# Optimization experiments

Hardware: AMD Instinct MI355X
Metric: run time of the kernel (lower is better)

The kernel has to match this reference:

```python
import jax, jax.numpy as jnp
import numpy as np

NUM_HEADS = 16
EPS = 1e-12  # torch F.normalize default eps


def _l2norm(t):
    n = jnp.linalg.norm(t, axis=-1, keepdims=True)
    return t / jnp.maximum(n, EPS)


def setup_inputs() -> dict:
    key = jax.random.key(0)
    ks = jax.random.split(key, 5)
    N, C, d = 16, 1024, 1024
    x = jax.random.normal(ks[0], (N, C, d), dtype=jnp.float32)
    Wq = jax.random.normal(ks[1], (d, d), dtype=jnp.float32) * 0.02
    Wk = jax.random.normal(ks[2], (d, d), dtype=jnp.float32) * 0.02
    Wv = jax.random.normal(ks[3], (d, d), dtype=jnp.float32) * 0.02
    Wo = jax.random.normal(ks[4], (d, d), dtype=jnp.float32) * 0.02
    norm_const = 0.5 * jnp.ones((1, NUM_HEADS, 1, 1), dtype=jnp.float32)
    return {"x": x, "Wq": Wq, "Wk": Wk, "Wv": Wv, "Wo": Wo, "norm_const": norm_const}


def reference(x, Wq, Wk, Wv, Wo, norm_const):
    # attn_type='cosine', causal=False branch of Attention.forward
    N, C, d = x.shape
    H = NUM_HEADS
    hd = d // H
    # torch nn.Linear(bias=False): y = x @ W.T ; split heads -> [N, H, C, hd]
    def proj(W):
        return (x @ W.T).reshape(N, C, H, hd).transpose(0, 2, 1, 3)
    q = _l2norm(proj(Wq))
    k = _l2norm(proj(Wk))
    v = proj(Wv)
    # values = values / C ** sigmoid(norm_const)  (per-head scalar)
    v = v / jnp.power(jnp.float32(C), jax.nn.sigmoid(norm_const))
    # linear-attention reordering: q @ (k^T @ v); kv is [N, H, hd, hd]
    kv = jnp.einsum('nhcd,nhce->nhde', k, v)
    attn = jnp.einsum('nhcd,nhde->nhce', q, kv)
    out = attn.transpose(0, 2, 1, 3).reshape(N, C, d)
    return out @ Wo.T
```

## Files before the change

kernel.cpp:

```cpp
#include <hip/hip_runtime.h>
#include <stdint.h>

typedef __attribute__((ext_vector_type(4))) float f32x4;
typedef __attribute__((ext_vector_type(8))) short bf16x8;
typedef __attribute__((ext_vector_type(4))) unsigned short u16x4;
typedef __attribute__((ext_vector_type(4))) unsigned int u32x4;

typedef __attribute__((address_space(3))) char lds_t;
typedef const __attribute__((address_space(1))) char gmem_t;

__device__ __forceinline__ float bf2f(unsigned short u) {
  union { unsigned int u; float f; } a; a.u = ((unsigned int)u) << 16; return a.f;
}
__device__ __forceinline__ unsigned short f2bf(float f) {
  union { float f; unsigned int u; } a; a.f = f;
  unsigned int r = a.u + 0x7fffu + ((a.u >> 16) & 1u);
  return (unsigned short)(r >> 16);
}

__global__ void cvt_kernel(const float* __restrict__ in, unsigned short* __restrict__ out, int n) {
  int i = (blockIdx.x * blockDim.x + threadIdx.x) * 8;
  if (i >= n) return;
  const f32x4 a = *(const f32x4*)(in + i);
  const f32x4 b = *(const f32x4*)(in + i + 4);
  alignas(16) unsigned short o[8];
#pragma unroll
  for (int k = 0; k < 4; ++k) { o[k] = f2bf(a[k]); o[4 + k] = f2bf(b[k]); }
  *(u32x4*)(out + i) = *(const u32x4*)o;
}

__global__ void cvtw_kernel(const float* __restrict__ W0, const float* __restrict__ W1,
                            const float* __restrict__ W2, const float* __restrict__ W3,
                            unsigned short* __restrict__ wqkv, unsigned short* __restrict__ wob) {
  const int s = blockIdx.y;
  const float* in = (s == 0) ? W0 : (s == 1) ? W1 : (s == 2) ? W2 : W3;
  unsigned short* out = (s < 3) ? (wqkv + s * 1048576) : wob;
  int i = (blockIdx.x * blockDim.x + threadIdx.x) * 8;
  const f32x4 a = *(const f32x4*)(in + i);
  const f32x4 b = *(const f32x4*)(in + i + 4);
  alignas(16) unsigned short o[8];
#pragma unroll
  for (int k = 0; k < 4; ++k) { o[k] = f2bf(a[k]); o[4 + k] = f2bf(b[k]); }
  *(u32x4*)(out + i) = *(const u32x4*)o;
}

template<int GX, int MODE>
__global__ __launch_bounds__(512, 2) void gemm256(
    const unsigned short* __restrict__ A, const unsigned short* __restrict__ B,
    void* __restrict__ O0, void* __restrict__ O1, void* __restrict__ O2,
    const float* __restrict__ nc)
{
  constexpr int K = 1024;
  constexpr int NT = K / 64;
  constexpr int NWG = GX * 64;
  constexpr int CPX = NWG >> 3;
  const int p = blockIdx.y * GX + blockIdx.x;
  const int lid = (p & 7) * CPX + (p >> 3);
  const int bm0 = (lid / GX) * 256;
  const int bn0 = (lid % GX) * 256;
  const int t = threadIdx.x;
  const int l = t & 63;
  const int w = t >> 6;
  const int wm = w >> 2;
  const int wn = w & 3;

  __shared__ char smem[131072];

  const int srow = t >> 3;
  const int schunk = t & 7;
  const int sck = schunk ^ (srow & 7);

#define STAGE_A(so_, kt_, lam_)                                                                  \
  __builtin_amdgcn_global_load_lds(                                                             \
      (gmem_t*)(A + (long long)(bm0 + (lam_) * 64 + srow) * K + (kt_) * 64 + sck * 8),          \
      (lds_t*)(smem + (so_) + ((lam_) * 64 + srow) * 128 + schunk * 16), 16, 0, 0)
#define STAGE_B(so_, kt_, lam_)                                                                  \
  __builtin_amdgcn_global_load_lds(                                                             \
      (gmem_t*)(B + (long long)(bn0 + (lam_) * 64 + srow) * K + (kt_) * 64 + sck * 8),          \
      (lds_t*)(smem + (so_) + 32768 + ((lam_) * 64 + srow) * 128 + schunk * 16), 16, 0, 0)

  const int xr = l & 7;
  const int chalf = l >> 4;
  int aoff[8], boff[4];
#pragma unroll
  for (int fr = 0; fr < 8; ++fr) aoff[fr] = (wm * 128 + fr * 16 + (l & 15)) * 128;
#pragma unroll
  for (int fc = 0; fc < 4; ++fc) boff[fc] = 32768 + (wn * 64 + fc * 16 + (l & 15)) * 128;

  f32x4 acc[8][4];
#pragma unroll
  for (int i = 0; i < 8; ++i)
#pragma unroll
    for (int j = 0; j < 4; ++j) acc[i][j] = f32x4{0.f, 0.f, 0.f, 0.f};

#pragma unroll
  for (int lam = 0; lam < 4; ++lam) STAGE_A(0, 0, lam);
#pragma unroll
  for (int lam = 0; lam < 4; ++lam) STAGE_B(0, 0, lam);
#pragma unroll
  for (int lam = 0; lam < 4; ++lam) STAGE_B(65536, 1, lam);
  asm volatile("s_waitcnt vmcnt(4)" ::: "memory");
  __builtin_amdgcn_s_barrier();
  __builtin_amdgcn_sched_barrier(0);

  for (int u = 0; u < NT; ++u) {
    const int slot = (u & 1) << 16;
    const int nslot = slot ^ 65536;
    bf16x8 bv[4][2];
#pragma unroll
    for (int q = 0; q < 4; ++q) {
      if (q == 0) {
#pragma unroll
        for (int j = 0; j < 4; ++j)
#pragma unroll
          for (int ks = 0; ks < 2; ++ks)
            bv[j][ks] = *(const bf16x8*)(smem + slot + boff[j] + (((ks * 4 + chalf) ^ xr) * 16));
      }
      bf16x8 av[2][2];
#pragma unroll
      for (int d = 0; d < 2; ++d)
#pragma unroll
        for (int ks = 0; ks < 2; ++ks)
          av[d][ks] = *(const bf16x8*)(smem + slot + aoff[2 * q + d] + (((ks * 4 + chalf) ^ xr) * 16));
      if (q == 0)      { if (u + 1 < NT) { STAGE_A(nslot, u + 1, 0); STAGE_A(nslot, u + 1, 1); } }
      else if (q == 1) { if (u + 1 < NT) { STAGE_A(nslot, u + 1, 2); STAGE_A(nslot, u + 1, 3); } }
      else if (q == 2) { if (u + 2 < NT) { STAGE_B(slot, u + 2, 0);  STAGE_B(slot, u + 2, 1); } }
      else             { if (u + 2 < NT) { STAGE_B(slot, u + 2, 2);  STAGE_B(slot, u + 2, 3); } }
      __builtin_amdgcn_s_barrier();
      asm volatile("s_waitcnt lgkmcnt(0)" ::: "memory");
      __builtin_amdgcn_sched_barrier(0);
      __builtin_amdgcn_s_setprio(1);
#pragma unroll
      for (int d = 0; d < 2; ++d)
#pragma unroll
        for (int j = 0; j < 4; ++j)
#pragma unroll
          for (int ks = 0; ks < 2; ++ks)
            acc[2 * q + d][j] =
                __builtin_amdgcn_mfma_f32_16x16x32_bf16(av[d][ks], bv[j][ks], acc[2 * q + d][j], 0, 0, 0);
      __builtin_amdgcn_s_setprio(0);
      if (q == 3) {
        if (u + 2 < NT) { asm volatile("s_waitcnt vmcnt(4)" ::: "memory"); }
        else            { asm volatile("s_waitcnt vmcnt(0)" ::: "memory"); }
      }
      __builtin_amdgcn_s_barrier();
      __builtin_amdgcn_sched_barrier(0);
    }
  }
#undef STAGE_A
#undef STAGE_B

  const int wcol0 = bn0 + wn * 64;
  const int rowb = bm0 + wm * 128 + (l >> 4) * 4;

  if (MODE == 0) {
    float* Op = (float*)O0;
    const int colb = wcol0 + (l & 15);
#pragma unroll
    for (int i = 0; i < 8; ++i)
#pragma unroll
      for (int j = 0; j < 4; ++j)
#pragma unroll
        for (int r = 0; r < 4; ++r)
          Op[(long long)(rowb + i * 16 + r) * 1024 + (colb + j * 16)] = acc[i][j][r];
  } else {
    const int sel = wcol0 >> 10;
    const int col_in = wcol0 & 1023;
    const int h = col_in >> 6;
    if (sel < 2) {
#pragma unroll
      for (int i = 0; i < 8; ++i)
#pragma unroll
        for (int r = 0; r < 4; ++r) {
          float s = 0.f;
#pragma unroll
          for (int j = 0; j < 4; ++j) s += acc[i][j][r] * acc[i][j][r];
          s += __shfl_xor(s, 1); s += __shfl_xor(s, 2);
          s += __shfl_xor(s, 4); s += __shfl_xor(s, 8);
          const float inv = 1.f / fmaxf(sqrtf(s), 1e-12f);
#pragma unroll
          for (int j = 0; j < 4; ++j) acc[i][j][r] *= inv;
        }
    } else {
      const float sig = 1.f / (1.f + expf(-nc[h]));
      const float vsc = expf(-6.9314718055994530942f * sig);
#pragma unroll
      for (int i = 0; i < 8; ++i)
#pragma unroll
        for (int j = 0; j < 4; ++j)
#pragma unroll
          for (int r = 0; r < 4; ++r) acc[i][j][r] *= vsc;
    }
    if (sel == 0) {
      unsigned short* Op = (unsigned short*)O0;
      const int colb = col_in + (l & 15);
#pragma unroll
      for (int i = 0; i < 8; ++i)
#pragma unroll
        for (int j = 0; j < 4; ++j)
#pragma unroll
          for (int r = 0; r < 4; ++r)
            Op[(long long)(rowb + i * 16 + r) * 1024 + (colb + j * 16)] = f2bf(acc[i][j][r]);
    } else {
      unsigned short* Tp = (unsigned short*)(sel == 1 ? O1 : O2)
                         + ((long long)((bm0 >> 10) * 16 + h) * 64) * 1024;
      const int c0 = (bm0 & 1023) + wm * 128 + (l >> 4) * 4;
#pragma unroll
      for (int i = 0; i < 8; ++i)
#pragma unroll
        for (int j = 0; j < 4; ++j)
#pragma unroll
          for (int r = 0; r < 4; ++r)
            Tp[(long long)(j * 16 + (l & 15)) * 1024 + (c0 + i * 16 + r)] = f2bf(acc[i][j][r]);
    }
  }
}

__global__ __launch_bounds__(256) void kv_mfma(
    const unsigned short* __restrict__ vT, const unsigned short* __restrict__ kT,
    unsigned short* __restrict__ kvT)
{
  const int h = blockIdx.x, n = blockIdx.y;
  const int t = threadIdx.x, l = t & 63, w = t >> 6;
  __shared__ char smem[131072];
  const long long base = (long long)(n * 16 + h) * 64 * 1024;
  const int srow = l >> 3;
  const int schunk = l & 7;
  char* wbuf = smem + w * 32768;

#define KV_STAGE(buf_, cc_) do {                                                                  \
    const int col_ = w * 256 + (cc_) * 64;                                                        \
    _Pragma("unroll")                                                                             \
    for (int i_ = 0; i_ < 8; ++i_) {                                                              \
      const int r_ = i_ * 8 + srow;                                                               \
      const int sc_ = schunk ^ srow;                                                              \
      __builtin_amdgcn_global_load_lds((gmem_t*)(vT + base + (long long)r_ * 1024 + col_ + sc_ * 8), \
                                       (lds_t*)((buf_) + r_ * 128 + schunk * 16), 16, 0, 0);      \
      __builtin_amdgcn_global_load_lds((gmem_t*)(kT + base + (long long)r_ * 1024 + col_ + sc_ * 8), \
                                       (lds_t*)((buf_) + 8192 + r_ * 128 + schunk * 16), 16, 0, 0); \
    }                                                                                             \
  } while (0)

  const int xr = l & 7, chalf = l >> 4;
  f32x4 acc[4][4];
#pragma unroll
  for (int i = 0; i < 4; ++i)
#pragma unroll
    for (int j = 0; j < 4; ++j) acc[i][j] = f32x4{0.f, 0.f, 0.f, 0.f};

  KV_STAGE(wbuf, 0);
  for (int cc = 0; cc < 4; ++cc) {
    char* cur = wbuf + (cc & 1) * 16384;
    if (cc < 3) {
      KV_STAGE(wbuf + ((cc + 1) & 1) * 16384, cc + 1);
      asm volatile("s_waitcnt vmcnt(16)" ::: "memory");
    } else {
      asm volatile("s_waitcnt vmcnt(0)" ::: "memory");
    }
    bf16x8 av[4][2], bvv[4][2];
#pragma unroll
    for (int m = 0; m < 4; ++m)
#pragma unroll
      for (int ks = 0; ks < 2; ++ks) {
        const int ch = ((ks * 4 + chalf) ^ xr) * 16;
        av[m][ks]  = *(const bf16x8*)(cur + (m * 16 + (l & 15)) * 128 + ch);
        bvv[m][ks] = *(const bf16x8*)(cur + 8192 + (m * 16 + (l & 15)) * 128 + ch);
      }
#pragma unroll
    for (int m = 0; m < 4; ++m)
#pragma unroll
      for (int j = 0; j < 4; ++j)
#pragma unroll
        for (int ks = 0; ks < 2; ++ks)
          acc[m][j] = __builtin_amdgcn_mfma_f32_16x16x32_bf16(av[m][ks], bvv[j][ks], acc[m][j], 0, 0, 0);
  }
#undef KV_STAGE

  __syncthreads();
  float* red = (float*)smem;
#pragma unroll
  for (int m = 0; m < 4; ++m)
#pragma unroll
    for (int j = 0; j < 4; ++j)
      *(f32x4*)&red[w * 4096 + (m * 4 + j) * 256 + l * 4] = acc[m][j];
  __syncthreads();

  const int e = t >> 2, d0 = (t & 3) * 16;
  const int m = e >> 4, rr = e & 3, lhi = (e & 15) >> 2;
  alignas(16) unsigned short o16[16];
#pragma unroll
  for (int dd = 0; dd < 16; ++dd) {
    const int d = d0 + dd;
    const int f = m * 4 + (d >> 4);
    const int pos = (lhi * 16 + (d & 15)) * 4 + rr;
    float s = red[f * 256 + pos] + red[4096 + f * 256 + pos] +
              red[8192 + f * 256 + pos] + red[12288 + f * 256 + pos];
    o16[dd] = f2bf(s);
  }
  unsigned short* dst = kvT + (long long)(n * 16 + h) * 4096 + e * 64 + d0;
  *(u32x4*)dst = *(const u32x4*)&o16[0];
  *((u32x4*)dst + 1) = *(const u32x4*)&o16[8];
}

__global__ __launch_bounds__(256) void attn_mfma(
    unsigned short* __restrict__ q, const unsigned short* __restrict__ kvT)
{
  const int ct = blockIdx.x, h = blockIdx.y, n = blockIdx.z;
  const int t = threadIdx.x, l = t & 63, w = t >> 6;
  __shared__ char smem[40960];
  const long long R0 = (long long)n * 1024 + ct * 256;
  {
    const int sr = t >> 3;
    const int sc = (t & 7) ^ (sr & 7);
#pragma unroll
    for (int i = 0; i < 8; ++i) {
      const int r = i * 32 + sr;
      __builtin_amdgcn_global_load_lds((gmem_t*)(q + (R0 + r) * 1024 + h * 64 + sc * 8),
                                       (lds_t*)(smem + r * 128 + (t & 7) * 16), 16, 0, 0);
    }
#pragma unroll
    for (int i = 0; i < 2; ++i) {
      const int r = i * 32 + sr;
      __builtin_amdgcn_global_load_lds((gmem_t*)(kvT + (long long)(n * 16 + h) * 4096 + r * 64 + sc * 8),
                                       (lds_t*)(smem + 32768 + r * 128 + (t & 7) * 16), 16, 0, 0);
    }
  }
  asm volatile("s_waitcnt vmcnt(0)" ::: "memory");
  __syncthreads();

  const int xr = l & 7, chalf = l >> 4;
  f32x4 acc[4][4];
#pragma unroll
  for (int i = 0; i < 4; ++i)
#pragma unroll
    for (int j = 0; j < 4; ++j) acc[i][j] = f32x4{0.f, 0.f, 0.f, 0.f};
  bf16x8 av[4][2], bvv[4][2];
#pragma unroll
  for (int m = 0; m < 4; ++m)
#pragma unroll
    for (int ks = 0; ks < 2; ++ks) {
      const int ch = ((ks * 4 + chalf) ^ xr) * 16;
      av[m][ks]  = *(const bf16x8*)(smem + (w * 64 + m * 16 + (l & 15)) * 128 + ch);
      bvv[m][ks] = *(const bf16x8*)(smem + 32768 + (m * 16 + (l & 15)) * 128 + ch);
    }
#pragma unroll
  for (int m = 0; m < 4; ++m)
#pragma unroll
    for (int j = 0; j < 4; ++j)
#pragma unroll
      for (int ks = 0; ks < 2; ++ks)
        acc[m][j] = __builtin_amdgcn_mfma_f32_16x16x32_bf16(av[m][ks], bvv[j][ks], acc[m][j], 0, 0, 0);

  const int rb = w * 64 + (l >> 4) * 4;
#pragma unroll
  for (int m = 0; m < 4; ++m)
#pragma unroll
    for (int j = 0; j < 4; ++j)
#pragma unroll
      for (int r = 0; r < 4; ++r)
        q[(R0 + rb + m * 16 + r) * 1024 + h * 64 + j * 16 + (l & 15)] = f2bf(acc[m][j][r]);
}

extern "C" void kernel_launch(void* const* d_in, const int* in_sizes, int n_in,
                              void* d_out, int out_size, void* d_ws, size_t ws_size,
                              hipStream_t stream) {
  (void)in_sizes; (void)n_in; (void)out_size; (void)ws_size;
  const float* x  = (const float*)d_in[0];
  const float* Wq = (const float*)d_in[1];
  const float* Wk = (const float*)d_in[2];
  const float* Wv = (const float*)d_in[3];
  const float* Wo = (const float*)d_in[4];
  const float* nc = (const float*)d_in[5];

  unsigned short* xb  = (unsigned short*)d_out;
  unsigned short* kvT = (unsigned short*)((char*)d_out + 33554432ll);

  char* ws = (char*)d_ws;
  unsigned short* wqkv = (unsigned short*)ws;
  unsigned short* wob  = wqkv + 3 * 1048576;
  unsigned short* qb   = wob + 1048576;
  unsigned short* kTb  = qb + 16777216;
  unsigned short* vTb  = kTb + 16777216;

  cvt_kernel<<<8192, 256, 0, stream>>>(x, xb, 16777216);
  cvtw_kernel<<<dim3(512, 4), 256, 0, stream>>>(Wq, Wk, Wv, Wo, wqkv, wob);

  gemm256<12, 1><<<dim3(12, 64), 512, 0, stream>>>(xb, wqkv, qb, kTb, vTb, nc);
  kv_mfma<<<dim3(16, 16), 256, 0, stream>>>(vTb, kTb, kvT);
  attn_mfma<<<dim3(4, 16, 16), 256, 0, stream>>>(qb, kvT);
  gemm256<4, 0><<<dim3(4, 64), 512, 0, stream>>>(qb, wob, d_out, nullptr, nullptr, nullptr);
}
```

Baseline: 209.4 us.

## Stage GEMM epilogues through LDS for coalesced stores and merge conversion kernels

The GEMM epilogues now write the accumulators into shared memory first, then each thread writes full 16-byte vectors to global memory. This covers the fp32 output, the row-major bf16 Q output and the transposed bf16 K/V outputs. It replaces scattered 2- and 4-byte per-lane stores, most of all the strided transposed writes. Shared memory grows to hold a padded 256x256 bf16 tile, and extra barriers are added. The x and weight fp32→bf16 conversion kernels are also merged into one launch to save launch overhead.

```diff
diff --git a/kernel.cpp b/kernel.cpp
--- a/kernel.cpp
+++ b/kernel.cpp
@@ -18,30 +18,31 @@
   return (unsigned short)(r >> 16);
 }
 
-__global__ void cvt_kernel(const float* __restrict__ in, unsigned short* __restrict__ out, int n) {
-  int i = (blockIdx.x * blockDim.x + threadIdx.x) * 8;
-  if (i >= n) return;
-  const f32x4 a = *(const f32x4*)(in + i);
-  const f32x4 b = *(const f32x4*)(in + i + 4);
+__global__ __launch_bounds__(256) void cvt_all(
+    const float* __restrict__ x, const float* __restrict__ W0, const float* __restrict__ W1,
+    const float* __restrict__ W2, const float* __restrict__ W3,
+    unsigned short* __restrict__ xb, unsigned short* __restrict__ wqkv,
+    unsigned short* __restrict__ wob)
+{
+  const int b = blockIdx.x;
+  const float* src;
+  unsigned short* dst;
+  int i;
+  if (b < 8192) {
+    src = x; dst = xb; i = b * 2048 + threadIdx.x * 8;
+  } else {
+    const int s = (b - 8192) >> 9;
+    const int bb = (b - 8192) & 511;
+    i = bb * 2048 + threadIdx.x * 8;
+    src = (s == 0) ? W0 : (s == 1) ? W1 : (s == 2) ? W2 : W3;
+    dst = (s < 3) ? (wqkv + s * 1048576) : wob;
+  }
+  const f32x4 a = *(const f32x4*)(src + i);
+  const f32x4 c = *(const f32x4*)(src + i + 4);
   alignas(16) unsigned short o[8];
 #pragma unroll
-  for (int k = 0; k < 4; ++k) { o[k] = f2bf(a[k]); o[4 + k] = f2bf(b[k]); }
-  *(u32x4*)(out + i) = *(const u32x4*)o;
-}
-
-__global__ void cvtw_kernel(const float* __restrict__ W0, const float* __restrict__ W1,
-                            const float* __restrict__ W2, const float* __restrict__ W3,
-                            unsigned short* __restrict__ wqkv, unsigned short* __restrict__ wob) {
-  const int s = blockIdx.y;
-  const float* in = (s == 0) ? W0 : (s == 1) ? W1 : (s == 2) ? W2 : W3;
-  unsigned short* out = (s < 3) ? (wqkv + s * 1048576) : wob;
-  int i = (blockIdx.x * blockDim.x + threadIdx.x) * 8;
-  const f32x4 a = *(const f32x4*)(in + i);
-  const f32x4 b = *(const f32x4*)(in + i + 4);
-  alignas(16) unsigned short o[8];
-#pragma unroll
-  for (int k = 0; k < 4; ++k) { o[k] = f2bf(a[k]); o[4 + k] = f2bf(b[k]); }
-  *(u32x4*)(out + i) = *(const u32x4*)o;
+  for (int k = 0; k < 4; ++k) { o[k] = f2bf(a[k]); o[4 + k] = f2bf(c[k]); }
+  *(u32x4*)(dst + i) = *(const u32x4*)o;
 }
 
 template<int GX, int MODE>
@@ -64,7 +65,7 @@
   const int wm = w >> 2;
   const int wn = w & 3;
 
-  __shared__ char smem[131072];
+  __shared__ char smem[143360];
 
   const int srow = t >> 3;
   const int schunk = t & 7;
@@ -151,18 +152,33 @@
 #undef STAGE_B
 
   const int wcol0 = bn0 + wn * 64;
-  const int rowb = bm0 + wm * 128 + (l >> 4) * 4;
+  const int rowb_l = wm * 128 + (l >> 4) * 4;
+  const int colb_l = wn * 64 + (l & 15);
 
   if (MODE == 0) {
-    float* Op = (float*)O0;
-    const int colb = wcol0 + (l & 15);
-#pragma unroll
-    for (int i = 0; i < 8; ++i)
-#pragma unroll
-      for (int j = 0; j < 4; ++j)
-#pragma unroll
-        for (int r = 0; r < 4; ++r)
-          Op[(long long)(rowb + i * 16 + r) * 1024 + (colb + j * 16)] = acc[i][j][r];
+    float* ldsf = (float*)smem;
+#pragma unroll
+    for (int hi = 0; hi < 2; ++hi) {
+      if (wm == hi) {
+#pragma unroll
+        for (int i = 0; i < 8; ++i)
+#pragma unroll
+          for (int j = 0; j < 4; ++j)
+#pragma unroll
+            for (int r = 0; r < 4; ++r)
+              ldsf[((l >> 4) * 4 + i * 16 + r) * 264 + colb_l + j * 16] = acc[i][j][r];
+      }
+      __syncthreads();
+      {
+        const int row = t & 127, cq = t >> 7;
+        float* dst = (float*)O0 + (long long)(bm0 + hi * 128 + row) * 1024 + bn0 + cq * 64;
+        const float* srcl = ldsf + row * 264 + cq * 64;
+#pragma unroll
+        for (int g = 0; g < 16; ++g)
+          *(f32x4*)(dst + g * 4) = *(const f32x4*)(srcl + g * 4);
+      }
+      __syncthreads();
+    }
   } else {
     const int sel = wcol0 >> 10;
     const int col_in = wcol0 & 1023;
@@ -191,27 +207,42 @@
 #pragma unroll
           for (int r = 0; r < 4; ++r) acc[i][j][r] *= vsc;
     }
+    unsigned short* lds16 = (unsigned short*)smem;
     if (sel == 0) {
-      unsigned short* Op = (unsigned short*)O0;
-      const int colb = col_in + (l & 15);
 #pragma unroll
       for (int i = 0; i < 8; ++i)
 #pragma unroll
         for (int j = 0; j < 4; ++j)
 #pragma unroll
           for (int r = 0; r < 4; ++r)
-            Op[(long long)(rowb + i * 16 + r) * 1024 + (colb + j * 16)] = f2bf(acc[i][j][r]);
+            lds16[(rowb_l + i * 16 + r) * 280 + colb_l + j * 16] = f2bf(acc[i][j][r]);
+      __syncthreads();
+      const int row = t & 255, half = t >> 8;
+      unsigned short* dst = (unsigned short*)O0 + (long long)(bm0 + row) * 1024 + bn0 + half * 128;
+      const unsigned short* srcl = lds16 + row * 280 + half * 128;
+#pragma unroll
+      for (int g = 0; g < 16; ++g)
+        *(u32x4*)(dst + g * 8) = *(const u32x4*)(srcl + g * 8);
     } else {
-      unsigned short* Tp = (unsigned short*)(sel == 1 ? O1 : O2)
-                         + ((long long)((bm0 >> 10) * 16 + h) * 64) * 1024;
-      const int c0 = (bm0 & 1023) + wm * 128 + (l >> 4) * 4;
 #pragma unroll
       for (int i = 0; i < 8; ++i)
 #pragma unroll
         for (int j = 0; j < 4; ++j)
 #pragma unroll
           for (int r = 0; r < 4; ++r)
-            Tp[(long long)(j * 16 + (l & 15)) * 1024 + (c0 + i * 16 + r)] = f2bf(acc[i][j][r]);
+            lds16[(colb_l + j * 16) * 280 + rowb_l + i * 16 + r] = f2bf(acc[i][j][r]);
+      __syncthreads();
+      const int d = t & 255, chalf = t >> 8;
+      const int hh = ((bn0 & 1023) + d) >> 6;
+      const int dg = ((bn0 & 1023) + d) & 63;
+      const int n = bm0 >> 10;
+      unsigned short* Tp = (unsigned short*)(sel == 1 ? O1 : O2);
+      unsigned short* dst = Tp + ((long long)((n * 16 + hh) * 64 + dg)) * 1024
+                          + (bm0 & 1023) + chalf * 128;
+      const unsigned short* srcl = lds16 + d * 280 + chalf * 128;
+#pragma unroll
+      for (int g = 0; g < 16; ++g)
+        *(u32x4*)(dst + g * 8) = *(const u32x4*)(srcl + g * 8);
     }
   }
 }
@@ -382,8 +413,7 @@
   unsigned short* kTb  = qb + 16777216;
   unsigned short* vTb  = kTb + 16777216;
 
-  cvt_kernel<<<8192, 256, 0, stream>>>(x, xb, 16777216);
-  cvtw_kernel<<<dim3(512, 4), 256, 0, stream>>>(Wq, Wk, Wv, Wo, wqkv, wob);
+  cvt_all<<<10240, 256, 0, stream>>>(x, Wq, Wk, Wv, Wo, xb, wqkv, wob);
 
   gemm256<12, 1><<<dim3(12, 64), 512, 0, stream>>>(xb, wqkv, qb, kTb, vTb, nc);
   kv_mfma<<<dim3(16, 16), 256, 0, stream>>>(vTb, kTb, kvT);
```

Result: slower. 231.3 us (+10.5%).
